# Optimization experiments

Hardware: AMD Instinct MI355X
Metric: run time of the kernel (lower is better)

## Reference

```python
import jax, jax.numpy as jnp
import numpy as np

B, T, D, H = 4, 2048, 256, 8
HD = D // H  # head_dim = 32
ALPHA_INIT = 0.5


def setup_inputs() -> dict:
    key = jax.random.key(0)
    ks = jax.random.split(key, 9)
    s = 1.0 / np.sqrt(D)
    inp = {
        "content": jax.random.normal(ks[0], (B, T, D), dtype=jnp.float32),
        "category": jax.random.normal(ks[1], (B, T, D), dtype=jnp.float32),
        "Wqc": jax.random.normal(ks[2], (D, D), dtype=jnp.float32) * s,
        "Wkc": jax.random.normal(ks[3], (D, D), dtype=jnp.float32) * s,
        "Wv": jax.random.normal(ks[4], (D, D), dtype=jnp.float32) * s,
        "Wqk": jax.random.normal(ks[5], (D, D), dtype=jnp.float32) * s,
        "Wkk": jax.random.normal(ks[6], (D, D), dtype=jnp.float32) * s,
        "Wo": jax.random.normal(ks[7], (D, D), dtype=jnp.float32) * s,
        "bo": jnp.zeros((D,), dtype=jnp.float32),
        "alpha_logit": jnp.float32(np.log(ALPHA_INIT / (1.0 - ALPHA_INIT))),
        "causal_mask": jnp.triu(jnp.ones((T, T), dtype=bool), k=1),  # True = blocked
    }
    return inp


def _split_heads(x):
    # [B, T, D] -> [B, H, T, HD]
    b, t, _ = x.shape
    return x.reshape(b, t, H, HD).transpose(0, 2, 1, 3)


def reference(content, category, Wqc, Wkc, Wv, Wqk, Wkk, Wo, bo, alpha_logit, causal_mask):
    scale = HD ** (-0.5)
    # torch nn.Linear(bias=False): y = x @ W.T
    Qc = _split_heads(content @ Wqc.T)
    Kc = _split_heads(content @ Wkc.T)
    V = _split_heads(content @ Wv.T)
    Qk = _split_heads(category @ Wqk.T)
    Kk = _split_heads(category @ Wkk.T)

    neg_inf = jnp.finfo(content.dtype).min
    Ac = jnp.einsum("bhqd,bhkd->bhqk", Qc, Kc) * scale
    Ak = jnp.einsum("bhqd,bhkd->bhqk", Qk, Kk) * scale
    Ac = jnp.where(causal_mask, neg_inf, Ac)
    Ak = jnp.where(causal_mask, neg_inf, Ak)
    Ac = jax.nn.softmax(Ac, axis=-1)
    Ak = jax.nn.softmax(Ak, axis=-1)

    alpha = jax.nn.sigmoid(alpha_logit)
    A = alpha * Ak + (1.0 - alpha) * Ac  # dropout is identity in eval mode

    out = jnp.einsum("bhqk,bhkd->bhqd", A, V)
    out = out.transpose(0, 2, 1, 3).reshape(content.shape[0], -1, D)
    return out @ Wo.T + bo
```

## Files before the change

### kernel.cpp

```cpp
#include <hip/hip_runtime.h>
#include <hip/hip_bf16.h>

#define Bb 4
#define Tt 2048
#define Dd 256
#define Hh 8
#define Mm (Bb * Tt)

typedef __attribute__((ext_vector_type(8))) short short8v;
typedef __attribute__((ext_vector_type(4))) short short4v;
typedef __attribute__((ext_vector_type(4))) float f32x4;
typedef __attribute__((ext_vector_type(4))) unsigned uint4v;

#define MFMA16(a, b, c) __builtin_amdgcn_mfma_f32_16x16x32_bf16(a, b, c, 0, 0, 0)

__device__ __forceinline__ void gload16(const void* g, void* l) {
  __builtin_amdgcn_global_load_lds((const __attribute__((address_space(1))) void*)g,
                                   (__attribute__((address_space(3))) void*)l, 16, 0, 0);
}

__device__ __forceinline__ short bfc(float f) {
  __hip_bfloat16 h = __float2bfloat16(f);
  return *reinterpret_cast<short*>(&h);
}
__device__ __forceinline__ unsigned pk2bf(float lo, float hi) {
  union { float f; unsigned u; } a, b; a.f = lo; b.f = hi;
  return __builtin_amdgcn_perm(b.u, a.u, 0x07060302u);
}

__global__ __launch_bounds__(256)
void proj_kernel(const float* __restrict__ content, const float* __restrict__ category,
                 const float* __restrict__ Wqc, const float* __restrict__ Wkc,
                 const float* __restrict__ Wv, const float* __restrict__ Wqk,
                 const float* __restrict__ Wkk, short* __restrict__ ws) {
  __shared__ short Al[128][40];
  __shared__ short Bl[128][40];

  const int mt = blockIdx.x;
  const int nt = blockIdx.y;
  const int p  = nt >> 1;
  const int n0 = (nt & 1) << 7;

  const float* X = (p < 3) ? content : category;
  const float* W = (p == 0) ? Wqc : (p == 1) ? Wkc : (p == 2) ? Wv : (p == 3) ? Wqk : Wkk;
  short* Y = ws + (size_t)p * ((size_t)Mm * Dd);
  const float oscale = (p == 0 || p == 3)
      ? (0.17677669529663689f * 1.4426950408889634f) : 1.0f;

  const int tid  = threadIdx.x;
  const int lane = tid & 63;
  const int wv   = tid >> 6;
  const int wm   = (wv >> 1) << 6;
  const int wn   = (wv & 1) << 6;
  const int l15  = lane & 15;
  const int l4   = lane >> 4;

  const f32x4 zero = {0.f, 0.f, 0.f, 0.f};
  f32x4 acc[4][4];
#pragma unroll
  for (int i = 0; i < 4; i++)
#pragma unroll
    for (int j = 0; j < 4; j++) acc[i][j] = zero;

  const int rs = tid >> 3;
  const int cs = (tid & 7) << 2;

  for (int k0 = 0; k0 < Dd; k0 += 32) {
#pragma unroll
    for (int pass = 0; pass < 4; pass++) {
      const int r = rs + (pass << 5);
      const float4 va = *reinterpret_cast<const float4*>(&X[(size_t)(mt * 128 + r) * Dd + k0 + cs]);
      short4v sa; sa[0] = bfc(va.x); sa[1] = bfc(va.y); sa[2] = bfc(va.z); sa[3] = bfc(va.w);
      *reinterpret_cast<short4v*>(&Al[r][cs]) = sa;
      const float4 vb = *reinterpret_cast<const float4*>(&W[(size_t)(n0 + r) * Dd + k0 + cs]);
      short4v sb; sb[0] = bfc(vb.x); sb[1] = bfc(vb.y); sb[2] = bfc(vb.z); sb[3] = bfc(vb.w);
      *reinterpret_cast<short4v*>(&Bl[r][cs]) = sb;
    }
    __syncthreads();

    short8v af[4], bfr[4];
#pragma unroll
    for (int i = 0; i < 4; i++)
      af[i] = *reinterpret_cast<const short8v*>(&Al[wm + i * 16 + l15][l4 * 8]);
#pragma unroll
    for (int j = 0; j < 4; j++)
      bfr[j] = *reinterpret_cast<const short8v*>(&Bl[wn + j * 16 + l15][l4 * 8]);
#pragma unroll
    for (int i = 0; i < 4; i++)
#pragma unroll
      for (int j = 0; j < 4; j++)
        acc[i][j] = MFMA16(af[i], bfr[j], acc[i][j]);
    __syncthreads();
  }

  if (p == 2) {
#pragma unroll
    for (int i = 0; i < 4; i++) {
      const int trow = mt * 128 + wm + i * 16 + (l4 << 2);
      const int bidx = trow >> 11;
      const int tloc = trow & 2047;
#pragma unroll
      for (int j = 0; j < 4; j++) {
        const int cg = n0 + wn + j * 16 + l15;
        const int hh = cg >> 5, dd2 = cg & 31;
        short4v pk;
#pragma unroll
        for (int e = 0; e < 4; e++) pk[e] = bfc(acc[i][j][e]);
        *reinterpret_cast<short4v*>(&Y[((size_t)(bidx * 8 + hh) * 32 + dd2) * Tt + tloc]) = pk;
      }
    }
  } else {
#pragma unroll
    for (int i = 0; i < 4; i++) {
      const int rb = mt * 128 + wm + i * 16 + (l4 << 2);
#pragma unroll
      for (int j = 0; j < 4; j++) {
        const int c = n0 + wn + j * 16 + l15;
#pragma unroll
        for (int e = 0; e < 4; e++)
          Y[(size_t)(rb + e) * Dd + c] = bfc(acc[i][j][e] * oscale);
      }
    }
  }
}

__global__ __launch_bounds__(512, 4)
void attn_kernel(const short* __restrict__ Qc, const short* __restrict__ Kc,
                 const short* __restrict__ Vt, const short* __restrict__ Qk,
                 const short* __restrict__ Kk, short* __restrict__ AO,
                 const float* __restrict__ alpha_p) {
  __shared__ __align__(16) char ldsraw[49152];

  const int bid = blockIdx.x;
  const int bh  = bid & 31;
  const int pr  = bid >> 5;
  const int qA  = pr, qB = 31 - pr;
  const int b = bh >> 3, h = bh & 7;
  const size_t rowbase = (size_t)b * Tt;
  const short* __restrict__ Vh  = Vt + (size_t)bh * 32 * Tt;
  const short* __restrict__ KcB = Kc + rowbase * Dd + h * 32;
  const short* __restrict__ KkB = Kk + rowbase * Dd + h * 32;

  const int tid  = threadIdx.x;
  const int lane = tid & 63;
  const int grp  = tid >> 8;
  const int tg   = tid & 255;
  const int wg   = (tid >> 6) & 3;
  const int l15  = lane & 15, g = lane >> 4;

  char* gb = ldsraw + grp * 24576;

  const int slot = tg >> 2;
  const int ksrc = ((slot >> 4) & 1) * 32 + ((slot >> 2) & 3) * 8
                 + (slot >> 5) * 4 + (slot & 3);
  const int kcg  = (tg & 3) ^ ((slot >> 1) & 3);
  const int vrow = tg >> 3;
  const int vcg  = (tg & 7) ^ (vrow & 7);

  const int koff  = l15 * 32 + ((g ^ ((l15 >> 1) & 3)) << 3);
  const int voff0 = l15 * 64 + (((g) ^ (l15 & 7)) << 3);
  const int voff1 = l15 * 64 + (((4 + g) ^ (l15 & 7)) << 3);

  const float alpha = 1.f / (1.f + __builtin_amdgcn_exp2f(-alpha_p[0] * 1.4426950408889634f));
  const f32x4 zf = {0.f, 0.f, 0.f, 0.f};

  const size_t qoffA = (rowbase + (qA << 6) + wg * 16 + l15) * (size_t)Dd + h * 32 + g * 8;
  const size_t qoffB = (rowbase + (qB << 6) + wg * 16 + l15) * (size_t)Dd + h * 32 + g * 8;
  const short8v qcA = *(const short8v*)&Qc[qoffA];
  const short8v qkA = *(const short8v*)&Qk[qoffA];
  const short8v qcB = *(const short8v*)&Qc[qoffB];
  const short8v qkB = *(const short8v*)&Qk[qoffB];

  f32x4 ov[2][2][2];
  float ls[2][2] = {{0.f, 0.f}, {0.f, 0.f}};
#pragma unroll
  for (int t = 0; t < 2; t++)
#pragma unroll
    for (int s = 0; s < 2; s++) { ov[t][s][0] = zf; ov[t][s][1] = zf; }

  {
    const size_t k0s = (size_t)(grp << 6);
    gload16(KcB + (k0s + ksrc) * Dd + kcg * 8, gb + wg * 1024);
    gload16(KkB + (k0s + ksrc) * Dd + kcg * 8, gb + 8192 + wg * 1024);
    gload16(Vh + (size_t)vrow * Tt + k0s + vcg * 8, gb + 16384 + wg * 1024);
  }
  __syncthreads();

  const short* kcPf = KcB + ((size_t)((grp + 2) << 6) + ksrc) * Dd + kcg * 8;
  const short* kkPf = KkB + ((size_t)((grp + 2) << 6) + ksrc) * Dd + kcg * 8;
  const short* vtPf = Vh + (size_t)vrow * Tt + ((grp + 2) << 6) + vcg * 8;
  const size_t kstep = (size_t)128 * Dd;

  const int nIter = (qB >> 1) + 1;
  int jt = grp;
  for (int it = 0; it < nIter; ++it, jt += 2) {
    const int cur = it & 1;
    if (jt + 2 <= qB) {
      char* db = gb + (cur ^ 1) * 4096 + wg * 1024;
      gload16(kcPf, db);
      gload16(kkPf, db + 8192);
      gload16(vtPf, db + 16384);
      kcPf += kstep; kkPf += kstep; vtPf += 128;
    }
    if (jt <= qB) {
      const short* kcl = (const short*)(gb + cur * 4096);
      const short* kkl = (const short*)(gb + 8192 + cur * 4096);
      const short* vtl = (const short*)(gb + 16384 + cur * 4096);

      const short8v vb00 = *(const short8v*)(vtl + voff0);
      const short8v vb10 = *(const short8v*)(vtl + voff0 + 1024);
      const short8v vb01 = *(const short8v*)(vtl + voff1);
      const short8v vb11 = *(const short8v*)(vtl + voff1 + 1024);

#pragma unroll
      for (int t = 0; t < 2; t++) {
        if (t == 0 && jt > qA) continue;
        const int qt = t ? qB : qA;
        const bool diag = (jt == qt);
        const bool full = !diag || (wg >= 2);
#pragma unroll
        for (int s = 0; s < 2; s++) {
          const short* kl = s ? kkl : kcl;
          const short8v qf = t ? (s ? qkB : qcB) : (s ? qkA : qcA);
          f32x4 sf[4];
#pragma unroll
          for (int f = 0; f < 4; f++) {
            if (((f & 1) == 0) || full) {
              const short8v kf = *(const short8v*)(kl + koff + f * 512);
              sf[f] = MFMA16(kf, qf, zf);
            }
          }
          if (diag) {
            const int thb = 16 * wg + l15 - 8 * g;
#pragma unroll
            for (int f = 0; f < 4; f++) {
              if (((f & 1) == 0) || full) {
                const int thr = thb - 32 * (f & 1) - 4 * (f >> 1);
#pragma unroll
                for (int e = 0; e < 4; e++)
                  if (e > thr) sf[f][e] = -1e30f;
              }
            }
          }
#pragma unroll
          for (int f = 0; f < 4; f++) {
            if (((f & 1) == 0) || full) {
#pragma unroll
              for (int e = 0; e < 4; e++)
                sf[f][e] = __builtin_amdgcn_exp2f(sf[f][e]);
            }
          }
          const float t0 = (sf[0][0] + sf[0][1]) + (sf[0][2] + sf[0][3]);
          const float t2 = (sf[2][0] + sf[2][1]) + (sf[2][2] + sf[2][3]);
          float ts = t0 + t2;
          if (full) {
            const float t1 = (sf[1][0] + sf[1][1]) + (sf[1][2] + sf[1][3]);
            const float t3 = (sf[3][0] + sf[3][1]) + (sf[3][2] + sf[3][3]);
            ts += (t1 + t3);
          }
          ts += __shfl_xor(ts, 16);
          ts += __shfl_xor(ts, 32);
          ls[t][s] += ts;

          union { uint4v u; short8v s8; } pa;
          pa.u = (uint4v){pk2bf(sf[0][0], sf[0][1]), pk2bf(sf[0][2], sf[0][3]),
                          pk2bf(sf[2][0], sf[2][1]), pk2bf(sf[2][2], sf[2][3])};
          __builtin_amdgcn_s_setprio(1);
          ov[t][s][0] = MFMA16(pa.s8, vb00, ov[t][s][0]);
          ov[t][s][1] = MFMA16(pa.s8, vb10, ov[t][s][1]);
          __builtin_amdgcn_s_setprio(0);
          if (full) {
            pa.u = (uint4v){pk2bf(sf[1][0], sf[1][1]), pk2bf(sf[1][2], sf[1][3]),
                            pk2bf(sf[3][0], sf[3][1]), pk2bf(sf[3][2], sf[3][3])};
            __builtin_amdgcn_s_setprio(1);
            ov[t][s][0] = MFMA16(pa.s8, vb01, ov[t][s][0]);
            ov[t][s][1] = MFMA16(pa.s8, vb11, ov[t][s][1]);
            __builtin_amdgcn_s_setprio(0);
          }
        }
      }
    }
    __syncthreads();
  }

  float* sp = (float*)ldsraw + (size_t)(wg * 64 + lane) * 40;
  if (grp == 1) {
#pragma unroll
    for (int t = 0; t < 2; t++)
#pragma unroll
      for (int s = 0; s < 2; s++) {
        *(f32x4*)(sp + (t * 2 + s) * 8)     = ov[t][s][0];
        *(f32x4*)(sp + (t * 2 + s) * 8 + 4) = ov[t][s][1];
      }
    sp[32] = ls[0][0]; sp[33] = ls[0][1];
    sp[34] = ls[1][0]; sp[35] = ls[1][1];
  }
  __syncthreads();
  if (grp == 0) {
#pragma unroll
    for (int t = 0; t < 2; t++) {
#pragma unroll
      for (int s = 0; s < 2; s++) {
        ov[t][s][0] += *(const f32x4*)(sp + (t * 2 + s) * 8);
        ov[t][s][1] += *(const f32x4*)(sp + (t * 2 + s) * 8 + 4);
      }
      const float l0 = ls[t][0] + sp[32 + t * 2];
      const float l1 = ls[t][1] + sp[33 + t * 2];
      float r0[4], r1[4];
#pragma unroll
      for (int e = 0; e < 4; e++) {
        r0[e] = (1.f - alpha) / __shfl(l0, 4 * g + e);
        r1[e] = alpha / __shfl(l1, 4 * g + e);
      }
      const size_t orow = rowbase + ((t ? qB : qA) << 6) + wg * 16 + g * 4;
#pragma unroll
      for (int n = 0; n < 2; n++)
#pragma unroll
        for (int e = 0; e < 4; e++) {
          const float o = ov[t][0][n][e] * r0[e] + ov[t][1][n][e] * r1[e];
          AO[(orow + e) * Dd + h * 32 + n * 16 + l15] = bfc(o);
        }
    }
  }
}

__global__ __launch_bounds__(256)
void outproj_kernel(const short* __restrict__ AO, const float* __restrict__ Wo,
                    const float* __restrict__ bo, float* __restrict__ out) {
  __shared__ short Al[64][40];
  __shared__ short Bl[64][40];

  const int mt = blockIdx.x;
  const int n0 = (int)blockIdx.y << 6;

  const int tid  = threadIdx.x;
  const int lane = tid & 63;
  const int wv   = tid >> 6;
  const int wm   = (wv >> 1) << 5;
  const int wn   = (wv & 1) << 5;
  const int l15  = lane & 15;
  const int g    = lane >> 4;

  const f32x4 zero = {0.f, 0.f, 0.f, 0.f};
  f32x4 acc[2][2] = {{zero, zero}, {zero, zero}};

  const int ra = tid >> 2, ca = (tid & 3) << 3;
  const int rb = tid >> 3, cb = (tid & 7) << 2;

  for (int k0 = 0; k0 < Dd; k0 += 32) {
    *reinterpret_cast<short8v*>(&Al[ra][ca]) =
        *reinterpret_cast<const short8v*>(&AO[(size_t)(mt * 64 + ra) * Dd + k0 + ca]);
#pragma unroll
    for (int pass = 0; pass < 2; pass++) {
      const int r = rb + (pass << 5);
      const float4 vb = *reinterpret_cast<const float4*>(&Wo[(size_t)(n0 + r) * Dd + k0 + cb]);
      short4v sb; sb[0] = bfc(vb.x); sb[1] = bfc(vb.y); sb[2] = bfc(vb.z); sb[3] = bfc(vb.w);
      *reinterpret_cast<short4v*>(&Bl[r][cb]) = sb;
    }
    __syncthreads();

    short8v af[2], bf2[2];
#pragma unroll
    for (int i = 0; i < 2; i++)
      af[i] = *reinterpret_cast<const short8v*>(&Al[wm + i * 16 + l15][g * 8]);
#pragma unroll
    for (int j = 0; j < 2; j++)
      bf2[j] = *reinterpret_cast<const short8v*>(&Bl[wn + j * 16 + l15][g * 8]);
#pragma unroll
    for (int i = 0; i < 2; i++)
#pragma unroll
      for (int j = 0; j < 2; j++)
        acc[i][j] = MFMA16(af[i], bf2[j], acc[i][j]);
    __syncthreads();
  }

#pragma unroll
  for (int i = 0; i < 2; i++) {
    const int r0w = mt * 64 + wm + i * 16 + (g << 2);
#pragma unroll
    for (int j = 0; j < 2; j++) {
      const int c = n0 + wn + j * 16 + l15;
      const float bias = bo[c];
#pragma unroll
      for (int e = 0; e < 4; e++)
        out[(size_t)(r0w + e) * Dd + c] = acc[i][j][e] + bias;
    }
  }
}

extern "C" void kernel_launch(void* const* d_in, const int* in_sizes, int n_in,
                              void* d_out, int out_size, void* d_ws, size_t ws_size,
                              hipStream_t stream) {
  const float* content = (const float*)d_in[0];
  const float* category = (const float*)d_in[1];
  const float* Wqc = (const float*)d_in[2];
  const float* Wkc = (const float*)d_in[3];
  const float* Wv  = (const float*)d_in[4];
  const float* Wqk = (const float*)d_in[5];
  const float* Wkk = (const float*)d_in[6];
  const float* Wo  = (const float*)d_in[7];
  const float* bo  = (const float*)d_in[8];
  const float* alpha_logit = (const float*)d_in[9];
  float* out = (float*)d_out;

  short* ws = (short*)d_ws;
  const size_t buf = (size_t)Mm * Dd;
  short* Qc = ws + 0 * buf;
  short* Kc = ws + 1 * buf;
  short* Vt = ws + 2 * buf;
  short* Qk = ws + 3 * buf;
  short* Kk = ws + 4 * buf;
  short* AO = ws + 5 * buf;

  proj_kernel<<<dim3(64, 10), 256, 0, stream>>>(content, category, Wqc, Wkc, Wv, Wqk, Wkk, ws);
  attn_kernel<<<dim3(512), 512, 0, stream>>>(Qc, Kc, Vt, Qk, Kk, AO, alpha_logit);
  outproj_kernel<<<dim3(128, 4), 256, 0, stream>>>(AO, Wo, bo, out);
}
```

Baseline: 70.17 us.

## Assign one query tile per attention block instead of paired tiles

The attention kernel stops pairing query tiles qA and 31-qA in one block and gives each block a single query tile, so the grid doubles to 1024 blocks. Tiles are ordered longest-first (qt = 31 - bid/32) so heavy blocks launch early. Register state per block is halved and launch bounds are raised to allow more resident blocks. In exchange, the K/V tiles below the diagonal are loaded once per query tile rather than shared across a pair, and per-block work becomes uneven.

```diff
diff --git a/kernel.cpp b/kernel.cpp
--- a/kernel.cpp
+++ b/kernel.cpp
@@ -124,7 +124,7 @@
   }
 }
 
-__global__ __launch_bounds__(512, 4)
+__global__ __launch_bounds__(512, 6)
 void attn_kernel(const short* __restrict__ Qc, const short* __restrict__ Kc,
                  const short* __restrict__ Vt, const short* __restrict__ Qk,
                  const short* __restrict__ Kk, short* __restrict__ AO,
@@ -133,8 +133,7 @@
 
   const int bid = blockIdx.x;
   const int bh  = bid & 31;
-  const int pr  = bid >> 5;
-  const int qA  = pr, qB = 31 - pr;
+  const int qt  = 31 - (bid >> 5);
   const int b = bh >> 3, h = bh & 7;
   const size_t rowbase = (size_t)b * Tt;
   const short* __restrict__ Vh  = Vt + (size_t)bh * 32 * Tt;
@@ -145,7 +144,7 @@
   const int lane = tid & 63;
   const int grp  = tid >> 8;
   const int tg   = tid & 255;
-  const int wg   = (tid >> 6) & 3;
+  const int wq   = (tid >> 6) & 3;
   const int l15  = lane & 15, g = lane >> 4;
 
   char* gb = ldsraw + grp * 24576;
@@ -164,25 +163,20 @@
   const float alpha = 1.f / (1.f + __builtin_amdgcn_exp2f(-alpha_p[0] * 1.4426950408889634f));
   const f32x4 zf = {0.f, 0.f, 0.f, 0.f};
 
-  const size_t qoffA = (rowbase + (qA << 6) + wg * 16 + l15) * (size_t)Dd + h * 32 + g * 8;
-  const size_t qoffB = (rowbase + (qB << 6) + wg * 16 + l15) * (size_t)Dd + h * 32 + g * 8;
-  const short8v qcA = *(const short8v*)&Qc[qoffA];
-  const short8v qkA = *(const short8v*)&Qk[qoffA];
-  const short8v qcB = *(const short8v*)&Qc[qoffB];
-  const short8v qkB = *(const short8v*)&Qk[qoffB];
-
-  f32x4 ov[2][2][2];
-  float ls[2][2] = {{0.f, 0.f}, {0.f, 0.f}};
-#pragma unroll
-  for (int t = 0; t < 2; t++)
-#pragma unroll
-    for (int s = 0; s < 2; s++) { ov[t][s][0] = zf; ov[t][s][1] = zf; }
+  const size_t qoff = (rowbase + (qt << 6) + wq * 16 + l15) * (size_t)Dd + h * 32 + g * 8;
+  const short8v qcf = *(const short8v*)&Qc[qoff];
+  const short8v qkf = *(const short8v*)&Qk[qoff];
+
+  f32x4 ov[2][2];
+  float ls[2] = {0.f, 0.f};
+#pragma unroll
+  for (int s = 0; s < 2; s++) { ov[s][0] = zf; ov[s][1] = zf; }
 
   {
     const size_t k0s = (size_t)(grp << 6);
-    gload16(KcB + (k0s + ksrc) * Dd + kcg * 8, gb + wg * 1024);
-    gload16(KkB + (k0s + ksrc) * Dd + kcg * 8, gb + 8192 + wg * 1024);
-    gload16(Vh + (size_t)vrow * Tt + k0s + vcg * 8, gb + 16384 + wg * 1024);
+    gload16(KcB + (k0s + ksrc) * Dd + kcg * 8, gb + wq * 1024);
+    gload16(KkB + (k0s + ksrc) * Dd + kcg * 8, gb + 8192 + wq * 1024);
+    gload16(Vh + (size_t)vrow * Tt + k0s + vcg * 8, gb + 16384 + wq * 1024);
   }
   __syncthreads();
 
@@ -191,18 +185,18 @@
   const short* vtPf = Vh + (size_t)vrow * Tt + ((grp + 2) << 6) + vcg * 8;
   const size_t kstep = (size_t)128 * Dd;
 
-  const int nIter = (qB >> 1) + 1;
+  const int nIter = (qt >> 1) + 1;
   int jt = grp;
   for (int it = 0; it < nIter; ++it, jt += 2) {
     const int cur = it & 1;
-    if (jt + 2 <= qB) {
-      char* db = gb + (cur ^ 1) * 4096 + wg * 1024;
+    if (jt + 2 <= qt) {
+      char* db = gb + (cur ^ 1) * 4096 + wq * 1024;
       gload16(kcPf, db);
       gload16(kkPf, db + 8192);
       gload16(vtPf, db + 16384);
       kcPf += kstep; kkPf += kstep; vtPf += 128;
     }
-    if (jt <= qB) {
+    if (jt <= qt) {
       const short* kcl = (const short*)(gb + cur * 4096);
       const short* kkl = (const short*)(gb + 8192 + cur * 4096);
       const short* vtl = (const short*)(gb + 16384 + cur * 4096);
@@ -212,115 +206,104 @@
       const short8v vb01 = *(const short8v*)(vtl + voff1);
       const short8v vb11 = *(const short8v*)(vtl + voff1 + 1024);
 
-#pragma unroll
-      for (int t = 0; t < 2; t++) {
-        if (t == 0 && jt > qA) continue;
-        const int qt = t ? qB : qA;
-        const bool diag = (jt == qt);
-        const bool full = !diag || (wg >= 2);
-#pragma unroll
-        for (int s = 0; s < 2; s++) {
-          const short* kl = s ? kkl : kcl;
-          const short8v qf = t ? (s ? qkB : qcB) : (s ? qkA : qcA);
-          f32x4 sf[4];
+      const bool diag = (jt == qt);
+      const bool full = !diag || (wq >= 2);
+#pragma unroll
+      for (int s = 0; s < 2; s++) {
+        const short* kl = s ? kkl : kcl;
+        const short8v qf = s ? qkf : qcf;
+        f32x4 sf[4];
+#pragma unroll
+        for (int f = 0; f < 4; f++) {
+          if (((f & 1) == 0) || full) {
+            const short8v kf = *(const short8v*)(kl + koff + f * 512);
+            sf[f] = MFMA16(kf, qf, zf);
+          }
+        }
+        if (diag) {
+          const int thb = 16 * wq + l15 - 8 * g;
 #pragma unroll
           for (int f = 0; f < 4; f++) {
             if (((f & 1) == 0) || full) {
-              const short8v kf = *(const short8v*)(kl + koff + f * 512);
-              sf[f] = MFMA16(kf, qf, zf);
+              const int thr = thb - 32 * (f & 1) - 4 * (f >> 1);
+#pragma unroll
+              for (int e = 0; e < 4; e++)
+                if (e > thr) sf[f][e] = -1e30f;
             }
           }
-          if (diag) {
-            const int thb = 16 * wg + l15 - 8 * g;
-#pragma unroll
-            for (int f = 0; f < 4; f++) {
-              if (((f & 1) == 0) || full) {
-                const int thr = thb - 32 * (f & 1) - 4 * (f >> 1);
-#pragma unroll
-                for (int e = 0; e < 4; e++)
-                  if (e > thr) sf[f][e] = -1e30f;
-              }
-            }
-          }
-#pragma unroll
-          for (int f = 0; f < 4; f++) {
-            if (((f & 1) == 0) || full) {
-#pragma unroll
-              for (int e = 0; e < 4; e++)
-                sf[f][e] = __builtin_amdgcn_exp2f(sf[f][e]);
-            }
-          }
-          const float t0 = (sf[0][0] + sf[0][1]) + (sf[0][2] + sf[0][3]);
-          const float t2 = (sf[2][0] + sf[2][1]) + (sf[2][2] + sf[2][3]);
-          float ts = t0 + t2;
-          if (full) {
-            const float t1 = (sf[1][0] + sf[1][1]) + (sf[1][2] + sf[1][3]);
-            const float t3 = (sf[3][0] + sf[3][1]) + (sf[3][2] + sf[3][3]);
-            ts += (t1 + t3);
-          }
-          ts += __shfl_xor(ts, 16);
-          ts += __shfl_xor(ts, 32);
-          ls[t][s] += ts;
-
-          union { uint4v u; short8v s8; } pa;
-          pa.u = (uint4v){pk2bf(sf[0][0], sf[0][1]), pk2bf(sf[0][2], sf[0][3]),
-                          pk2bf(sf[2][0], sf[2][1]), pk2bf(sf[2][2], sf[2][3])};
-          __builtin_amdgcn_s_setprio(1);
-          ov[t][s][0] = MFMA16(pa.s8, vb00, ov[t][s][0]);
-          ov[t][s][1] = MFMA16(pa.s8, vb10, ov[t][s][1]);
-          __builtin_amdgcn_s_setprio(0);
-          if (full) {
-            pa.u = (uint4v){pk2bf(sf[1][0], sf[1][1]), pk2bf(sf[1][2], sf[1][3]),
-                            pk2bf(sf[3][0], sf[3][1]), pk2bf(sf[3][2], sf[3][3])};
-            __builtin_amdgcn_s_setprio(1);
-            ov[t][s][0] = MFMA16(pa.s8, vb01, ov[t][s][0]);
-            ov[t][s][1] = MFMA16(pa.s8, vb11, ov[t][s][1]);
-            __builtin_amdgcn_s_setprio(0);
+        }
+#pragma unroll
+        for (int f = 0; f < 4; f++) {
+          if (((f & 1) == 0) || full) {
+#pragma unroll
+            for (int e = 0; e < 4; e++)
+              sf[f][e] = __builtin_amdgcn_exp2f(sf[f][e]);
           }
         }
+        const float t0 = (sf[0][0] + sf[0][1]) + (sf[0][2] + sf[0][3]);
+        const float t2 = (sf[2][0] + sf[2][1]) + (sf[2][2] + sf[2][3]);
+        float ts = t0 + t2;
+        if (full) {
+          const float t1 = (sf[1][0] + sf[1][1]) + (sf[1][2] + sf[1][3]);
+          const float t3 = (sf[3][0] + sf[3][1]) + (sf[3][2] + sf[3][3]);
+          ts += (t1 + t3);
+        }
+        ts += __shfl_xor(ts, 16);
+        ts += __shfl_xor(ts, 32);
+        ls[s] += ts;
+
+        union { uint4v u; short8v s8; } pa;
+        pa.u = (uint4v){pk2bf(sf[0][0], sf[0][1]), pk2bf(sf[0][2], sf[0][3]),
+                        pk2bf(sf[2][0], sf[2][1]), pk2bf(sf[2][2], sf[2][3])};
+        __builtin_amdgcn_s_setprio(1);
+        ov[s][0] = MFMA16(pa.s8, vb00, ov[s][0]);
+        ov[s][1] = MFMA16(pa.s8, vb10, ov[s][1]);
+        __builtin_amdgcn_s_setprio(0);
+        if (full) {
+          pa.u = (uint4v){pk2bf(sf[1][0], sf[1][1]), pk2bf(sf[1][2], sf[1][3]),
+                          pk2bf(sf[3][0], sf[3][1]), pk2bf(sf[3][2], sf[3][3])};
+          __builtin_amdgcn_s_setprio(1);
+          ov[s][0] = MFMA16(pa.s8, vb01, ov[s][0]);
+          ov[s][1] = MFMA16(pa.s8, vb11, ov[s][1]);
+          __builtin_amdgcn_s_setprio(0);
+        }
       }
     }
     __syncthreads();
   }
 
-  float* sp = (float*)ldsraw + (size_t)(wg * 64 + lane) * 40;
+  float* sp = (float*)ldsraw + (size_t)(wq * 64 + lane) * 20;
   if (grp == 1) {
 #pragma unroll
-    for (int t = 0; t < 2; t++)
-#pragma unroll
-      for (int s = 0; s < 2; s++) {
-        *(f32x4*)(sp + (t * 2 + s) * 8)     = ov[t][s][0];
-        *(f32x4*)(sp + (t * 2 + s) * 8 + 4) = ov[t][s][1];
-      }
-    sp[32] = ls[0][0]; sp[33] = ls[0][1];
-    sp[34] = ls[1][0]; sp[35] = ls[1][1];
+    for (int s = 0; s < 2; s++) {
+      *(f32x4*)(sp + s * 8)     = ov[s][0];
+      *(f32x4*)(sp + s * 8 + 4) = ov[s][1];
+    }
+    sp[16] = ls[0]; sp[17] = ls[1];
   }
   __syncthreads();
   if (grp == 0) {
 #pragma unroll
-    for (int t = 0; t < 2; t++) {
-#pragma unroll
-      for (int s = 0; s < 2; s++) {
-        ov[t][s][0] += *(const f32x4*)(sp + (t * 2 + s) * 8);
-        ov[t][s][1] += *(const f32x4*)(sp + (t * 2 + s) * 8 + 4);
+    for (int s = 0; s < 2; s++) {
+      ov[s][0] += *(const f32x4*)(sp + s * 8);
+      ov[s][1] += *(const f32x4*)(sp + s * 8 + 4);
+    }
+    const float l0 = ls[0] + sp[16];
+    const float l1 = ls[1] + sp[17];
+    float r0[4], r1[4];
+#pragma unroll
+    for (int e = 0; e < 4; e++) {
+      r0[e] = (1.f - alpha) / __shfl(l0, 4 * g + e);
+      r1[e] = alpha / __shfl(l1, 4 * g + e);
+    }
+    const size_t orow = rowbase + (qt << 6) + wq * 16 + g * 4;
+#pragma unroll
+    for (int n = 0; n < 2; n++)
+#pragma unroll
+      for (int e = 0; e < 4; e++) {
+        const float o = ov[0][n][e] * r0[e] + ov[1][n][e] * r1[e];
+        AO[(orow + e) * Dd + h * 32 + n * 16 + l15] = bfc(o);
       }
-      const float l0 = ls[t][0] + sp[32 + t * 2];
-      const float l1 = ls[t][1] + sp[33 + t * 2];
-      float r0[4], r1[4];
-#pragma unroll
-      for (int e = 0; e < 4; e++) {
-        r0[e] = (1.f - alpha) / __shfl(l0, 4 * g + e);
-        r1[e] = alpha / __shfl(l1, 4 * g + e);
-      }
-      const size_t orow = rowbase + ((t ? qB : qA) << 6) + wg * 16 + g * 4;
-#pragma unroll
-      for (int n = 0; n < 2; n++)
-#pragma unroll
-        for (int e = 0; e < 4; e++) {
-          const float o = ov[t][0][n][e] * r0[e] + ov[t][1][n][e] * r1[e];
-          AO[(orow + e) * Dd + h * 32 + n * 16 + l15] = bfc(o);
-        }
-    }
   }
 }
 
@@ -413,6 +396,6 @@
   short* AO = ws + 5 * buf;
 
   proj_kernel<<<dim3(64, 10), 256, 0, stream>>>(content, category, Wqc, Wkc, Wv, Wqk, Wkk, ws);
-  attn_kernel<<<dim3(512), 512, 0, stream>>>(Qc, Kc, Vt, Qk, Kk, AO, alpha_logit);
+  attn_kernel<<<dim3(1024), 512, 0, stream>>>(Qc, Kc, Vt, Qk, Kk, AO, alpha_logit);
   outproj_kernel<<<dim3(128, 4), 256, 0, stream>>>(AO, Wo, bo, out);
 }
```

Measured after the change: 116.3 us. 1.66x slower.
